# Performance work log

Hardware: AMD Instinct MI355X
Metric: run time of the kernel (lower is better)

The kernel has to match this reference:

```python
import jax, jax.numpy as jnp
import numpy as np

B, T, C, H, HS = 64, 128, 4096, 32, 128  # T must equal HS = C // H (source code constraint)
SCALE = 32.0 ** -0.5  # fixed constant in source, NOT head_size**-0.5


def setup_inputs() -> dict:
    key = jax.random.key(0)
    ks = jax.random.split(key, 6)
    s = 0.02
    return {
        "x": jax.random.normal(ks[0], (B, T, C), dtype=jnp.float32),
        "wq": jax.random.normal(ks[1], (H, C, HS), dtype=jnp.float32) * s,
        "wk": jax.random.normal(ks[2], (H, C, HS), dtype=jnp.float32) * s,
        "wv": jax.random.normal(ks[3], (H, C, HS), dtype=jnp.float32) * s,
        "wp": jax.random.normal(ks[4], (C, C), dtype=jnp.float32) * s,
        "bp": jnp.zeros((C,), dtype=jnp.float32),
    }


def reference(x, wq, wk, wv, wp, bp):
    # Batched per-head projections (source loops over heads; math identical).
    q = jnp.einsum("btc,hcs->bhts", x, wq)  # [B,H,T,HS]
    k = jnp.einsum("btc,hcs->bhts", x, wk)
    v = jnp.einsum("btc,hcs->bhts", x, wv)
    wei = jnp.einsum("bhts,bhus->bhtu", q, k) * SCALE  # [B,H,Tq,Tk]
    # Source uses F.softmax(wei, dim=1) on [B,Tq,Tk] -> softmax over QUERY axis.
    wei = jax.nn.softmax(wei, axis=2)
    out = jnp.einsum("bhtu,bhus->bhts", wei, v)  # [B,H,T,HS]
    # torch.cat(dim=1) over heads -> [B, H*T, HS]; then transpose(1,2) -> [B, HS, H*T]
    out = out.reshape(B, H * T, HS).transpose(0, 2, 1)  # [B, HS, H*T]; H*T == C
    out = jnp.einsum("bse,oe->bso", out, wp) + bp  # proj Linear
    return out  # dropout is identity in eval mode
```

## Files before the change

kernel.cpp:

```cpp
#include <hip/hip_runtime.h>
#include <cstddef>
#include <cstdint>

#define NB 64
#define NH 32
#define NT 128
#define NHS 128
#define NC 4096
#define SCALE 0.17677669529663687f
#define SLD 136

typedef __bf16 bf16_t;
typedef __bf16 bf16x8 __attribute__((ext_vector_type(8)));
typedef float  f32x4  __attribute__((ext_vector_type(4)));

__device__ __forceinline__ void load_lds16(const bf16_t* g, bf16_t* l) {
    __builtin_amdgcn_global_load_lds(
        (const __attribute__((address_space(1))) char*)g,
        (__attribute__((address_space(3))) char*)l,
        16, 0, 0);
}

__global__ __launch_bounds__(256) void cvt_bf16_kernel(
    const float* __restrict__ in, bf16_t* __restrict__ out, int n8)
{
    int i = blockIdx.x * 256 + threadIdx.x;
    if (i >= n8) return;
    const float4* p = (const float4*)in + (size_t)i * 2;
    float4 a = p[0], b = p[1];
    bf16x8 o;
    o[0] = (bf16_t)a.x; o[1] = (bf16_t)a.y; o[2] = (bf16_t)a.z; o[3] = (bf16_t)a.w;
    o[4] = (bf16_t)b.x; o[5] = (bf16_t)b.y; o[6] = (bf16_t)b.z; o[7] = (bf16_t)b.w;
    ((bf16x8*)out)[i] = o;
}

__global__ __launch_bounds__(256) void cvt_w_transpose_kernel(
    const float* __restrict__ wq, const float* __restrict__ wk, const float* __restrict__ wv,
    bf16_t* __restrict__ qt, bf16_t* __restrict__ kt, bf16_t* __restrict__ vt)
{
    const float* w; bf16_t* o;
    if (blockIdx.y == 0)      { w = wq; o = qt; }
    else if (blockIdx.y == 1) { w = wk; o = kt; }
    else                      { w = wv; o = vt; }
    const int h   = blockIdx.x >> 7;
    const int rem = blockIdx.x & 127;
    const int c0  = (rem >> 1) * 64;
    const int s0  = (rem & 1) * 64;
    const float* W = w + (size_t)h * NC * NHS;
    bf16_t* O = o + (size_t)h * NHS * NC;

    __shared__ float t[64][65];
    const int tid = threadIdx.x;
    #pragma unroll
    for (int it = 0; it < 16; ++it) {
        int idx = it * 256 + tid;
        int r = idx >> 6, cc = idx & 63;
        t[r][cc] = W[(size_t)(c0 + r) * NHS + s0 + cc];
    }
    __syncthreads();
    #pragma unroll
    for (int it = 0; it < 16; ++it) {
        int idx = it * 256 + tid;
        int sr = idx >> 6, cr = idx & 63;
        O[(size_t)(s0 + sr) * NC + c0 + cr] = (bf16_t)t[cr][sr];
    }
}

#define TILE_EL 16384

__device__ __forceinline__ void gemm256_core(
    const bf16_t* __restrict__ A, const bf16_t* __restrict__ BT, f32x4 acc[8][4])
{
    __shared__ __align__(16) bf16_t As[2 * TILE_EL];
    __shared__ __align__(16) bf16_t Bs[2 * TILE_EL];

    const int tid  = threadIdx.x;
    const int lane = tid & 63;
    const int w    = tid >> 6;
    const int wr   = w >> 2;
    const int wc   = w & 3;

    const int srow  = tid >> 3;
    const int scol  = ((tid & 7) * 8) ^ (((tid >> 3) & 7) << 3);
    const int sslot = tid * 8;

    const int frow = lane & 15;
    const int fk   = (lane >> 4) * 8;
    int aoff[2][2][4];
    #pragma unroll
    for (int ks = 0; ks < 2; ++ks)
        #pragma unroll
        for (int mh = 0; mh < 2; ++mh)
            #pragma unroll
            for (int q = 0; q < 4; ++q) {
                int r = wr * 128 + mh * 64 + q * 16 + frow;
                aoff[ks][mh][q] = r * 64 + ((ks * 32 + fk) ^ ((r & 7) << 3));
            }
    int boff[2][4];
    #pragma unroll
    for (int ks = 0; ks < 2; ++ks)
        #pragma unroll
        for (int n = 0; n < 4; ++n) {
            int r = wc * 64 + n * 16 + frow;
            boff[ks][n] = r * 64 + ((ks * 32 + fk) ^ ((r & 7) << 3));
        }

    auto stage = [&](const bf16_t* __restrict__ G, int half, int k0, bf16_t* dst) {
        #pragma unroll
        for (int jj = 0; jj < 2; ++jj) {
            const int j = half * 2 + jj;
            load_lds16(G + (size_t)(j * 64 + srow) * NC + (k0 + scol),
                       dst + j * 4096 + sslot);
        }
    };

    stage(A,  0, 0, As);           stage(A,  1, 0, As);
    stage(BT, 0, 0, Bs);           stage(BT, 1, 0, Bs);
    stage(A,  0, 64, As + TILE_EL); stage(A,  1, 64, As + TILE_EL);
    stage(BT, 0, 64, Bs + TILE_EL); stage(BT, 1, 64, Bs + TILE_EL);
    asm volatile("s_waitcnt vmcnt(8)" ::: "memory");
    __builtin_amdgcn_s_barrier();
    __builtin_amdgcn_sched_barrier(0);

    for (int t = 0; t < NC / 64; ++t) {
        bf16_t* Ac = As + (t & 1) * TILE_EL;
        bf16_t* Bc = Bs + (t & 1) * TILE_EL;
        const int  kn = t * 64 + 128;
        const bool pf = (t < NC / 64 - 2);

        bf16x8 b0[4], b1[4], a[4];
        #pragma unroll
        for (int n = 0; n < 4; ++n) b0[n] = *(const bf16x8*)(Bc + boff[0][n]);
        #pragma unroll
        for (int n = 0; n < 4; ++n) b1[n] = *(const bf16x8*)(Bc + boff[1][n]);
        #pragma unroll
        for (int q = 0; q < 4; ++q) a[q] = *(const bf16x8*)(Ac + aoff[0][0][q]);
        __builtin_amdgcn_s_setprio(1);
        #pragma unroll
        for (int q = 0; q < 4; ++q)
            #pragma unroll
            for (int n = 0; n < 4; ++n)
                acc[q][n] = __builtin_amdgcn_mfma_f32_16x16x32_bf16(a[q], b0[n], acc[q][n], 0, 0, 0);
        __builtin_amdgcn_s_setprio(0);
        asm volatile("s_waitcnt lgkmcnt(0)" ::: "memory");
        __builtin_amdgcn_s_barrier();
        __builtin_amdgcn_sched_barrier(0);

        if (pf) stage(BT, 0, kn, Bc);
        #pragma unroll
        for (int q = 0; q < 4; ++q) a[q] = *(const bf16x8*)(Ac + aoff[0][1][q]);
        __builtin_amdgcn_s_setprio(1);
        #pragma unroll
        for (int q = 0; q < 4; ++q)
            #pragma unroll
            for (int n = 0; n < 4; ++n)
                acc[4 + q][n] = __builtin_amdgcn_mfma_f32_16x16x32_bf16(a[q], b0[n], acc[4 + q][n], 0, 0, 0);
        __builtin_amdgcn_s_setprio(0);

        if (pf) stage(BT, 1, kn, Bc);
        #pragma unroll
        for (int q = 0; q < 4; ++q) a[q] = *(const bf16x8*)(Ac + aoff[1][0][q]);
        __builtin_amdgcn_s_setprio(1);
        #pragma unroll
        for (int q = 0; q < 4; ++q)
            #pragma unroll
            for (int n = 0; n < 4; ++n)
                acc[q][n] = __builtin_amdgcn_mfma_f32_16x16x32_bf16(a[q], b1[n], acc[q][n], 0, 0, 0);
        __builtin_amdgcn_s_setprio(0);

        #pragma unroll
        for (int q = 0; q < 4; ++q) a[q] = *(const bf16x8*)(Ac + aoff[1][1][q]);
        __builtin_amdgcn_s_setprio(1);
        #pragma unroll
        for (int q = 0; q < 4; ++q)
            #pragma unroll
            for (int n = 0; n < 4; ++n)
                acc[4 + q][n] = __builtin_amdgcn_mfma_f32_16x16x32_bf16(a[q], b1[n], acc[4 + q][n], 0, 0, 0);
        __builtin_amdgcn_s_setprio(0);

        asm volatile("s_waitcnt lgkmcnt(0)" ::: "memory");
        __builtin_amdgcn_s_barrier();
        __builtin_amdgcn_sched_barrier(0);
        if (pf) {
            stage(A, 0, kn, Ac); stage(A, 1, kn, Ac);
            asm volatile("s_waitcnt vmcnt(8)" ::: "memory");
        } else if (t == NC / 64 - 2) {
            asm volatile("s_waitcnt vmcnt(0)" ::: "memory");
        }
        __builtin_amdgcn_s_barrier();
        __builtin_amdgcn_sched_barrier(0);
    }
}

__global__ __launch_bounds__(512, 2) void qkv_gemm256_kernel(
    const bf16_t* __restrict__ xb, const bf16_t* __restrict__ wcat,
    bf16_t* __restrict__ q, bf16_t* __restrict__ k, bf16_t* __restrict__ v)
{
    const int bid = blockIdx.x;
    const int wg  = (bid & 7) * 192 + (bid >> 3);
    const int mt  = wg / 48;
    const int nt  = wg - mt * 48;
    const int Mb  = mt << 8;
    const int Nb  = nt << 8;

    f32x4 acc[8][4] = {};
    gemm256_core(xb + (size_t)Mb * NC, wcat + (size_t)Nb * NC, acc);

    const int tid = threadIdx.x, lane = tid & 63, w = tid >> 6;
    const int wr = w >> 2, wc = w & 3;
    const int tens = Nb >> 12;
    bf16_t* const outp = (tens == 0) ? q : (tens == 1) ? k : v;
    const int colb = Nb + wc * 64 + (lane & 15);
    const int rowb = Mb + wr * 128 + ((lane >> 4) << 2);
    #pragma unroll
    for (int i = 0; i < 8; ++i)
        #pragma unroll
        for (int r = 0; r < 4; ++r) {
            const int m  = rowb + i * 16 + r;
            const int bb = m >> 7, tt = m & 127;
            #pragma unroll
            for (int n = 0; n < 4; ++n) {
                const int ng = colb + n * 16;
                const int hh = (ng >> 7) & 31, ss = ng & 127;
                const size_t base = (size_t)((bb << 5) + hh) << 14;
                if (tens == 2) outp[base + ss * NT  + tt] = (bf16_t)acc[i][n][r];
                else           outp[base + tt * NHS + ss] = (bf16_t)acc[i][n][r];
            }
        }
}

__global__ __launch_bounds__(512, 2) void proj_gemm256_kernel(
    const bf16_t* __restrict__ attnT, const bf16_t* __restrict__ wpb,
    const float* __restrict__ bp, float* __restrict__ out)
{
    const int bid = blockIdx.x;
    const int wg  = (bid & 7) * 64 + (bid >> 3);
    const int mt  = wg >> 4;
    const int nt  = wg & 15;
    const int Mb  = mt << 8;
    const int Nb  = nt << 8;

    f32x4 acc[8][4] = {};
    gemm256_core(attnT + (size_t)Mb * NC, wpb + (size_t)Nb * NC, acc);

    const int tid = threadIdx.x, lane = tid & 63, w = tid >> 6;
    const int wr = w >> 2, wc = w & 3;
    const int colb = Nb + wc * 64 + (lane & 15);
    const int rowb = Mb + wr * 128 + ((lane >> 4) << 2);
    float bias[4];
    #pragma unroll
    for (int n = 0; n < 4; ++n) bias[n] = bp[colb + n * 16];
    #pragma unroll
    for (int i = 0; i < 8; ++i)
        #pragma unroll
        for (int r = 0; r < 4; ++r) {
            const size_t m = (size_t)(rowb + i * 16 + r);
            #pragma unroll
            for (int n = 0; n < 4; ++n)
                out[m * NC + colb + n * 16] = acc[i][n][r] + bias[n];
        }
}

__global__ __launch_bounds__(256) void attn_mfma_kernel(
    const bf16_t* __restrict__ q, const bf16_t* __restrict__ k,
    const bf16_t* __restrict__ vT, bf16_t* __restrict__ attnT)
{
    __shared__ __align__(16) bf16_t As[128 * 32];
    __shared__ __align__(16) bf16_t Bs[128 * 32];
    __shared__ __align__(16) bf16_t S[NT * SLD];

    const int bh = blockIdx.x;
    const int b = bh >> 5, h = bh & 31;
    const bf16_t* Q  = q  + (size_t)bh * NT * NHS;
    const bf16_t* K  = k  + (size_t)bh * NT * NHS;
    const bf16_t* VT = vT + (size_t)bh * NT * NHS;

    const int tid  = threadIdx.x;
    const int lane = tid & 63;
    const int wave = tid >> 6;
    const int wr = (wave >> 1) * 64;
    const int wc = (wave & 1) * 64;
    const int srow = tid >> 2;
    const int scol = (tid & 3) * 8;
    const int m0 = wr + (lane & 15);
    const int n0 = wc + (lane & 15);
    const int kq = (lane >> 4) * 8;
    const int rbase = wr + (lane >> 4) * 4;

    f32x4 acc[4][4] = {};

    for (int k0 = 0; k0 < NHS; k0 += 32) {
        load_lds16(Q + (size_t)srow        * NHS + k0 + scol, &As[srow * 32 + scol]);
        load_lds16(Q + (size_t)(srow + 64) * NHS + k0 + scol, &As[(srow + 64) * 32 + scol]);
        load_lds16(K + (size_t)srow        * NHS + k0 + scol, &Bs[srow * 32 + scol]);
        load_lds16(K + (size_t)(srow + 64) * NHS + k0 + scol, &Bs[(srow + 64) * 32 + scol]);
        __syncthreads();
        bf16x8 af[4], bfr[4];
        #pragma unroll
        for (int i = 0; i < 4; ++i) af[i]  = *(const bf16x8*)&As[(m0 + i * 16) * 32 + kq];
        #pragma unroll
        for (int j = 0; j < 4; ++j) bfr[j] = *(const bf16x8*)&Bs[(n0 + j * 16) * 32 + kq];
        #pragma unroll
        for (int i = 0; i < 4; ++i)
            #pragma unroll
            for (int j = 0; j < 4; ++j)
                acc[i][j] = __builtin_amdgcn_mfma_f32_16x16x32_bf16(af[i], bfr[j], acc[i][j], 0, 0, 0);
        __syncthreads();
    }
    #pragma unroll
    for (int i = 0; i < 4; ++i)
        #pragma unroll
        for (int j = 0; j < 4; ++j)
            #pragma unroll
            for (int r = 0; r < 4; ++r)
                S[(rbase + i * 16 + r) * SLD + wc + j * 16 + (lane & 15)] =
                    (bf16_t)(acc[i][j][r] * SCALE);
    __syncthreads();

    if (tid < NT) {
        const int u = tid;
        float m = -1e30f;
        for (int t = 0; t < NT; ++t) m = fmaxf(m, (float)S[t * SLD + u]);
        float sum = 0.f;
        for (int t = 0; t < NT; ++t) sum += __expf((float)S[t * SLD + u] - m);
        const float inv = 1.0f / sum;
        for (int t = 0; t < NT; ++t)
            S[t * SLD + u] = (bf16_t)(__expf((float)S[t * SLD + u] - m) * inv);
    }
    __syncthreads();

    #pragma unroll
    for (int i = 0; i < 4; ++i)
        #pragma unroll
        for (int j = 0; j < 4; ++j)
            acc[i][j] = (f32x4)(0.0f);

    for (int k0 = 0; k0 < NT; k0 += 32) {
        load_lds16(VT + (size_t)srow        * NT + k0 + scol, &As[srow * 32 + scol]);
        load_lds16(VT + (size_t)(srow + 64) * NT + k0 + scol, &As[(srow + 64) * 32 + scol]);
        __syncthreads();
        bf16x8 af[4], bfr[4];
        #pragma unroll
        for (int i = 0; i < 4; ++i) af[i]  = *(const bf16x8*)&As[(m0 + i * 16) * 32 + kq];
        #pragma unroll
        for (int j = 0; j < 4; ++j) bfr[j] = *(const bf16x8*)&S[(n0 + j * 16) * SLD + k0 + kq];
        #pragma unroll
        for (int i = 0; i < 4; ++i)
            #pragma unroll
            for (int j = 0; j < 4; ++j)
                acc[i][j] = __builtin_amdgcn_mfma_f32_16x16x32_bf16(af[i], bfr[j], acc[i][j], 0, 0, 0);
        __syncthreads();
    }
    bf16_t* AT = attnT + (size_t)b * NHS * NC + h * NT;
    #pragma unroll
    for (int i = 0; i < 4; ++i)
        #pragma unroll
        for (int j = 0; j < 4; ++j)
            #pragma unroll
            for (int r = 0; r < 4; ++r)
                AT[(size_t)(rbase + i * 16 + r) * NC + wc + j * 16 + (lane & 15)] =
                    (bf16_t)acc[i][j][r];
}

extern "C" void kernel_launch(void* const* d_in, const int* in_sizes, int n_in,
                              void* d_out, int out_size, void* d_ws, size_t ws_size,
                              hipStream_t stream) {
    const float* x  = (const float*)d_in[0];
    const float* wq = (const float*)d_in[1];
    const float* wk = (const float*)d_in[2];
    const float* wv = (const float*)d_in[3];
    const float* wp = (const float*)d_in[4];
    const float* bp = (const float*)d_in[5];
    float* out = (float*)d_out;

    const size_t NX = (size_t)NB * NT * NC;
    const size_t NW = (size_t)NH * NC * NHS;
    bf16_t* xb  = (bf16_t*)d_ws;
    bf16_t* wqT = xb  + NX;
    bf16_t* wkT = wqT + NW;
    bf16_t* wvT = wkT + NW;
    bf16_t* wpb = wvT + NW;
    bf16_t* qb  = wpb + NW;
    bf16_t* kb  = qb  + NX;
    bf16_t* vb  = kb  + NX;
    bf16_t* atT = vb  + NX;

    cvt_bf16_kernel<<<(int)(NX / 8 / 256), 256, 0, stream>>>(x, xb, (int)(NX / 8));
    cvt_w_transpose_kernel<<<dim3(4096, 3), 256, 0, stream>>>(wq, wk, wv, wqT, wkT, wvT);
    cvt_bf16_kernel<<<(int)(NW / 8 / 256), 256, 0, stream>>>(wp, wpb, (int)(NW / 8));

    qkv_gemm256_kernel<<<1536, 512, 0, stream>>>(xb, wqT, qb, kb, vb);
    attn_mfma_kernel<<<NB * NH, 256, 0, stream>>>(qb, kb, vb, atT);
    proj_gemm256_kernel<<<512, 512, 0, stream>>>(atT, wpb, bp, out);
}
```

Baseline: 1.648 ms.

## Triple-buffer A tiles and restructure GEMM loop into barrier-separated phases

Result: faster. 1.597 ms (-3.1%).

```diff
diff --git a/kernel.cpp b/kernel.cpp
--- a/kernel.cpp
+++ b/kernel.cpp
@@ -66,13 +66,13 @@
     }
 }
 
-#define TILE_EL 16384
+#define KT_EL 16384
 
 __device__ __forceinline__ void gemm256_core(
     const bf16_t* __restrict__ A, const bf16_t* __restrict__ BT, f32x4 acc[8][4])
 {
-    __shared__ __align__(16) bf16_t As[2 * TILE_EL];
-    __shared__ __align__(16) bf16_t Bs[2 * TILE_EL];
+    __shared__ __align__(16) bf16_t As[3 * KT_EL];
+    __shared__ __align__(16) bf16_t Bs[2 * KT_EL];
 
     const int tid  = threadIdx.x;
     const int lane = tid & 63;
@@ -90,11 +90,11 @@
     #pragma unroll
     for (int ks = 0; ks < 2; ++ks)
         #pragma unroll
-        for (int mh = 0; mh < 2; ++mh)
+        for (int ih = 0; ih < 2; ++ih)
             #pragma unroll
             for (int q = 0; q < 4; ++q) {
-                int r = wr * 128 + mh * 64 + q * 16 + frow;
-                aoff[ks][mh][q] = r * 64 + ((ks * 32 + fk) ^ ((r & 7) << 3));
+                int r = wr * 128 + ih * 64 + q * 16 + frow;
+                aoff[ks][ih][q] = r * 64 + ((ks * 32 + fk) ^ ((r & 7) << 3));
             }
     int boff[2][4];
     #pragma unroll
@@ -105,7 +105,7 @@
             boff[ks][n] = r * 64 + ((ks * 32 + fk) ^ ((r & 7) << 3));
         }
 
-    auto stage = [&](const bf16_t* __restrict__ G, int half, int k0, bf16_t* dst) {
+    auto stageH = [&](const bf16_t* __restrict__ G, int half, int k0, bf16_t* dst) {
         #pragma unroll
         for (int jj = 0; jj < 2; ++jj) {
             const int j = half * 2 + jj;
@@ -114,27 +114,37 @@
         }
     };
 
-    stage(A,  0, 0, As);           stage(A,  1, 0, As);
-    stage(BT, 0, 0, Bs);           stage(BT, 1, 0, Bs);
-    stage(A,  0, 64, As + TILE_EL); stage(A,  1, 64, As + TILE_EL);
-    stage(BT, 0, 64, Bs + TILE_EL); stage(BT, 1, 64, Bs + TILE_EL);
-    asm volatile("s_waitcnt vmcnt(8)" ::: "memory");
+    stageH(BT, 0, 0, Bs);          stageH(BT, 1, 0, Bs);
+    stageH(A,  0, 0, As);          stageH(A,  1, 0, As);
+    stageH(A,  0, 64, As + KT_EL); stageH(A,  1, 64, As + KT_EL);
+    asm volatile("s_waitcnt vmcnt(4)" ::: "memory");
     __builtin_amdgcn_s_barrier();
     __builtin_amdgcn_sched_barrier(0);
 
+    int a_cur = 0;
+    #pragma unroll 1
     for (int t = 0; t < NC / 64; ++t) {
-        bf16_t* Ac = As + (t & 1) * TILE_EL;
-        bf16_t* Bc = Bs + (t & 1) * TILE_EL;
-        const int  kn = t * 64 + 128;
-        const bool pf = (t < NC / 64 - 2);
-
-        bf16x8 b0[4], b1[4], a[4];
+        bf16_t* Ac = As + a_cur * KT_EL;
+        bf16_t* Bc = Bs + (t & 1) * KT_EL;
+        bf16_t* Bn = Bs + ((t + 1) & 1) * KT_EL;
+        const int a_n2 = (a_cur >= 1) ? a_cur - 1 : 2;
+        bf16_t* An = As + a_n2 * KT_EL;
+        const bool pfB = (t < NC / 64 - 1);
+        const bool pfA = (t < NC / 64 - 2);
+        const int kB = (t + 1) * 64;
+        const int kA = (t + 2) * 64;
+
+        bf16x8 a[4], b0[4], b1[4];
+
         #pragma unroll
         for (int n = 0; n < 4; ++n) b0[n] = *(const bf16x8*)(Bc + boff[0][n]);
         #pragma unroll
-        for (int n = 0; n < 4; ++n) b1[n] = *(const bf16x8*)(Bc + boff[1][n]);
-        #pragma unroll
         for (int q = 0; q < 4; ++q) a[q] = *(const bf16x8*)(Ac + aoff[0][0][q]);
+        if (pfB) stageH(BT, 0, kB, Bn);
+        __builtin_amdgcn_sched_barrier(0);
+        __builtin_amdgcn_s_barrier();
+        asm volatile("s_waitcnt lgkmcnt(0)" ::: "memory");
+        __builtin_amdgcn_sched_barrier(0);
         __builtin_amdgcn_s_setprio(1);
         #pragma unroll
         for (int q = 0; q < 4; ++q)
@@ -142,13 +152,16 @@
             for (int n = 0; n < 4; ++n)
                 acc[q][n] = __builtin_amdgcn_mfma_f32_16x16x32_bf16(a[q], b0[n], acc[q][n], 0, 0, 0);
         __builtin_amdgcn_s_setprio(0);
+        __builtin_amdgcn_s_barrier();
+        __builtin_amdgcn_sched_barrier(0);
+
+        #pragma unroll
+        for (int q = 0; q < 4; ++q) a[q] = *(const bf16x8*)(Ac + aoff[0][1][q]);
+        if (pfB) stageH(BT, 1, kB, Bn);
+        __builtin_amdgcn_sched_barrier(0);
+        __builtin_amdgcn_s_barrier();
         asm volatile("s_waitcnt lgkmcnt(0)" ::: "memory");
-        __builtin_amdgcn_s_barrier();
-        __builtin_amdgcn_sched_barrier(0);
-
-        if (pf) stage(BT, 0, kn, Bc);
-        #pragma unroll
-        for (int q = 0; q < 4; ++q) a[q] = *(const bf16x8*)(Ac + aoff[0][1][q]);
+        __builtin_amdgcn_sched_barrier(0);
         __builtin_amdgcn_s_setprio(1);
         #pragma unroll
         for (int q = 0; q < 4; ++q)
@@ -156,10 +169,18 @@
             for (int n = 0; n < 4; ++n)
                 acc[4 + q][n] = __builtin_amdgcn_mfma_f32_16x16x32_bf16(a[q], b0[n], acc[4 + q][n], 0, 0, 0);
         __builtin_amdgcn_s_setprio(0);
-
-        if (pf) stage(BT, 1, kn, Bc);
+        __builtin_amdgcn_s_barrier();
+        __builtin_amdgcn_sched_barrier(0);
+
+        #pragma unroll
+        for (int n = 0; n < 4; ++n) b1[n] = *(const bf16x8*)(Bc + boff[1][n]);
         #pragma unroll
         for (int q = 0; q < 4; ++q) a[q] = *(const bf16x8*)(Ac + aoff[1][0][q]);
+        if (pfA) stageH(A, 0, kA, An);
+        __builtin_amdgcn_sched_barrier(0);
+        __builtin_amdgcn_s_barrier();
+        asm volatile("s_waitcnt lgkmcnt(0)" ::: "memory");
+        __builtin_amdgcn_sched_barrier(0);
         __builtin_amdgcn_s_setprio(1);
         #pragma unroll
         for (int q = 0; q < 4; ++q)
@@ -167,9 +188,21 @@
             for (int n = 0; n < 4; ++n)
                 acc[q][n] = __builtin_amdgcn_mfma_f32_16x16x32_bf16(a[q], b1[n], acc[q][n], 0, 0, 0);
         __builtin_amdgcn_s_setprio(0);
+        __builtin_amdgcn_s_barrier();
+        __builtin_amdgcn_sched_barrier(0);
 
         #pragma unroll
         for (int q = 0; q < 4; ++q) a[q] = *(const bf16x8*)(Ac + aoff[1][1][q]);
+        if (pfA) {
+            stageH(A, 1, kA, An);
+            asm volatile("s_waitcnt vmcnt(4)" ::: "memory");
+        } else if (pfB) {
+            asm volatile("s_waitcnt vmcnt(0)" ::: "memory");
+        }
+        __builtin_amdgcn_sched_barrier(0);
+        __builtin_amdgcn_s_barrier();
+        asm volatile("s_waitcnt lgkmcnt(0)" ::: "memory");
+        __builtin_amdgcn_sched_barrier(0);
         __builtin_amdgcn_s_setprio(1);
         #pragma unroll
         for (int q = 0; q < 4; ++q)
@@ -177,18 +210,10 @@
             for (int n = 0; n < 4; ++n)
                 acc[4 + q][n] = __builtin_amdgcn_mfma_f32_16x16x32_bf16(a[q], b1[n], acc[4 + q][n], 0, 0, 0);
         __builtin_amdgcn_s_setprio(0);
-
-        asm volatile("s_waitcnt lgkmcnt(0)" ::: "memory");
-        __builtin_amdgcn_s_barrier();
-        __builtin_amdgcn_sched_barrier(0);
-        if (pf) {
-            stage(A, 0, kn, Ac); stage(A, 1, kn, Ac);
-            asm volatile("s_waitcnt vmcnt(8)" ::: "memory");
-        } else if (t == NC / 64 - 2) {
-            asm volatile("s_waitcnt vmcnt(0)" ::: "memory");
-        }
-        __builtin_amdgcn_s_barrier();
-        __builtin_amdgcn_sched_barrier(0);
+        __builtin_amdgcn_s_barrier();
+        __builtin_amdgcn_sched_barrier(0);
+
+        a_cur = (a_cur == 2) ? 0 : a_cur + 1;
     }
 }
 
```

## Restructure GEMM main loop into four-phase ping-pong schedule and vectorize V stores

Applied to the files above, without the earlier changes.

Measured after the change: 1.659 ms. About the same (+0.7%).

```diff
diff --git a/kernel.cpp b/kernel.cpp
--- a/kernel.cpp
+++ b/kernel.cpp
@@ -20,6 +20,10 @@
         (__attribute__((address_space(3))) char*)l,
         16, 0, 0);
 }
+
+#define SBAR() __builtin_amdgcn_sched_barrier(0)
+#define BARRIER() __builtin_amdgcn_s_barrier()
+#define LGKM0() asm volatile("s_waitcnt lgkmcnt(0)" ::: "memory")
 
 __global__ __launch_bounds__(256) void cvt_bf16_kernel(
     const float* __restrict__ in, bf16_t* __restrict__ out, int n8)
@@ -66,13 +70,13 @@
     }
 }
 
-#define TILE_EL 16384
+#define KT_EL 16384
 
 __device__ __forceinline__ void gemm256_core(
     const bf16_t* __restrict__ A, const bf16_t* __restrict__ BT, f32x4 acc[8][4])
 {
-    __shared__ __align__(16) bf16_t As[2 * TILE_EL];
-    __shared__ __align__(16) bf16_t Bs[2 * TILE_EL];
+    __shared__ __align__(16) bf16_t As[2 * KT_EL];
+    __shared__ __align__(16) bf16_t Bs[2 * KT_EL];
 
     const int tid  = threadIdx.x;
     const int lane = tid & 63;
@@ -90,11 +94,11 @@
     #pragma unroll
     for (int ks = 0; ks < 2; ++ks)
         #pragma unroll
-        for (int mh = 0; mh < 2; ++mh)
+        for (int ih = 0; ih < 2; ++ih)
             #pragma unroll
             for (int q = 0; q < 4; ++q) {
-                int r = wr * 128 + mh * 64 + q * 16 + frow;
-                aoff[ks][mh][q] = r * 64 + ((ks * 32 + fk) ^ ((r & 7) << 3));
+                int r = wr * 128 + ih * 64 + q * 16 + frow;
+                aoff[ks][ih][q] = r * 64 + ((ks * 32 + fk) ^ ((r & 7) << 3));
             }
     int boff[2][4];
     #pragma unroll
@@ -105,90 +109,148 @@
             boff[ks][n] = r * 64 + ((ks * 32 + fk) ^ ((r & 7) << 3));
         }
 
-    auto stage = [&](const bf16_t* __restrict__ G, int half, int k0, bf16_t* dst) {
-        #pragma unroll
-        for (int jj = 0; jj < 2; ++jj) {
-            const int j = half * 2 + jj;
-            load_lds16(G + (size_t)(j * 64 + srow) * NC + (k0 + scol),
-                       dst + j * 4096 + sslot);
-        }
+    auto stageS = [&](const bf16_t* __restrict__ G, int j, int k0, bf16_t* dst) {
+        load_lds16(G + (size_t)(j * 64 + srow) * NC + (k0 + scol),
+                   dst + j * 4096 + sslot);
     };
-
-    stage(A,  0, 0, As);           stage(A,  1, 0, As);
-    stage(BT, 0, 0, Bs);           stage(BT, 1, 0, Bs);
-    stage(A,  0, 64, As + TILE_EL); stage(A,  1, 64, As + TILE_EL);
-    stage(BT, 0, 64, Bs + TILE_EL); stage(BT, 1, 64, Bs + TILE_EL);
-    asm volatile("s_waitcnt vmcnt(8)" ::: "memory");
-    __builtin_amdgcn_s_barrier();
-    __builtin_amdgcn_sched_barrier(0);
-
-    for (int t = 0; t < NC / 64; ++t) {
-        bf16_t* Ac = As + (t & 1) * TILE_EL;
-        bf16_t* Bc = Bs + (t & 1) * TILE_EL;
-        const int  kn = t * 64 + 128;
-        const bool pf = (t < NC / 64 - 2);
-
-        bf16x8 b0[4], b1[4], a[4];
-        #pragma unroll
-        for (int n = 0; n < 4; ++n) b0[n] = *(const bf16x8*)(Bc + boff[0][n]);
-        #pragma unroll
-        for (int n = 0; n < 4; ++n) b1[n] = *(const bf16x8*)(Bc + boff[1][n]);
-        #pragma unroll
-        for (int q = 0; q < 4; ++q) a[q] = *(const bf16x8*)(Ac + aoff[0][0][q]);
+    auto stageH = [&](const bf16_t* __restrict__ G, int half, int k0, bf16_t* dst) {
+        #pragma unroll
+        for (int jj = 0; jj < 2; ++jj)
+            stageS(G, half * 2 + jj, k0, dst);
+    };
+
+    stageH(A,  0, 0, As);  stageH(A,  1, 0, As);
+    stageH(BT, 0, 0, Bs);  stageH(BT, 1, 0, Bs);
+    stageS(A, 0, 64, As + KT_EL);
+    stageS(A, 2, 64, As + KT_EL);
+    stageH(BT, 0, 64, Bs + KT_EL);
+    stageH(BT, 1, 64, Bs + KT_EL);
+    asm volatile("s_waitcnt vmcnt(6)" ::: "memory");
+    BARRIER();
+    SBAR();
+
+    bf16x8 b0c[2][2];
+    #pragma unroll
+    for (int ks = 0; ks < 2; ++ks)
+        #pragma unroll
+        for (int n = 0; n < 2; ++n)
+            b0c[ks][n] = *(const bf16x8*)(Bs + boff[ks][n]);
+
+    #pragma unroll 1
+    for (int t = 0; t < 64; ++t) {
+        const int p = t & 1;
+        bf16_t* Ac = As + p * KT_EL;
+        bf16_t* Bc = Bs + p * KT_EL;
+        bf16_t* Ao = As + (p ^ 1) * KT_EL;
+        bf16_t* Bo = Bs + (p ^ 1) * KT_EL;
+        const bool s1 = (t < 63);
+        const bool s2 = (t < 62);
+        const int k1 = (t + 1) * 64;
+        const int k2 = (t + 2) * 64;
+
+        bf16x8 a0[2][4], a1[2][4], b1[2][2], b0n[2][2];
+
+        #pragma unroll
+        for (int ks = 0; ks < 2; ++ks)
+            #pragma unroll
+            for (int q = 0; q < 4; ++q)
+                a0[ks][q] = *(const bf16x8*)(Ac + aoff[ks][0][q]);
+        if (s1) { stageS(A, 1, k1, Ao); stageS(A, 3, k1, Ao); }
+        SBAR();
+        BARRIER();
+        LGKM0();
+        SBAR();
         __builtin_amdgcn_s_setprio(1);
         #pragma unroll
-        for (int q = 0; q < 4; ++q)
-            #pragma unroll
-            for (int n = 0; n < 4; ++n)
-                acc[q][n] = __builtin_amdgcn_mfma_f32_16x16x32_bf16(a[q], b0[n], acc[q][n], 0, 0, 0);
+        for (int ks = 0; ks < 2; ++ks)
+            #pragma unroll
+            for (int q = 0; q < 4; ++q)
+                #pragma unroll
+                for (int n = 0; n < 2; ++n)
+                    acc[q][n] = __builtin_amdgcn_mfma_f32_16x16x32_bf16(a0[ks][q], b0c[ks][n], acc[q][n], 0, 0, 0);
         __builtin_amdgcn_s_setprio(0);
-        asm volatile("s_waitcnt lgkmcnt(0)" ::: "memory");
-        __builtin_amdgcn_s_barrier();
-        __builtin_amdgcn_sched_barrier(0);
-
-        if (pf) stage(BT, 0, kn, Bc);
-        #pragma unroll
-        for (int q = 0; q < 4; ++q) a[q] = *(const bf16x8*)(Ac + aoff[0][1][q]);
+        BARRIER();
+        SBAR();
+
+        #pragma unroll
+        for (int ks = 0; ks < 2; ++ks)
+            #pragma unroll
+            for (int n = 0; n < 2; ++n)
+                b1[ks][n] = *(const bf16x8*)(Bc + boff[ks][2 + n]);
+        if (s2) { stageS(A, 0, k2, Ac); stageS(A, 2, k2, Ac); }
+        SBAR();
+        BARRIER();
+        LGKM0();
+        SBAR();
         __builtin_amdgcn_s_setprio(1);
         #pragma unroll
-        for (int q = 0; q < 4; ++q)
-            #pragma unroll
-            for (int n = 0; n < 4; ++n)
-                acc[4 + q][n] = __builtin_amdgcn_mfma_f32_16x16x32_bf16(a[q], b0[n], acc[4 + q][n], 0, 0, 0);
+        for (int ks = 0; ks < 2; ++ks)
+            #pragma unroll
+            for (int q = 0; q < 4; ++q)
+                #pragma unroll
+                for (int n = 0; n < 2; ++n)
+                    acc[q][2 + n] = __builtin_amdgcn_mfma_f32_16x16x32_bf16(a0[ks][q], b1[ks][n], acc[q][2 + n], 0, 0, 0);
         __builtin_amdgcn_s_setprio(0);
-
-        if (pf) stage(BT, 1, kn, Bc);
-        #pragma unroll
-        for (int q = 0; q < 4; ++q) a[q] = *(const bf16x8*)(Ac + aoff[1][0][q]);
+        BARRIER();
+        SBAR();
+
+        #pragma unroll
+        for (int ks = 0; ks < 2; ++ks)
+            #pragma unroll
+            for (int q = 0; q < 4; ++q)
+                a1[ks][q] = *(const bf16x8*)(Ac + aoff[ks][1][q]);
+        if (s2) stageH(BT, 0, k2, Bc);
+        SBAR();
+        BARRIER();
+        LGKM0();
+        SBAR();
         __builtin_amdgcn_s_setprio(1);
         #pragma unroll
-        for (int q = 0; q < 4; ++q)
-            #pragma unroll
-            for (int n = 0; n < 4; ++n)
-                acc[q][n] = __builtin_amdgcn_mfma_f32_16x16x32_bf16(a[q], b1[n], acc[q][n], 0, 0, 0);
+        for (int ks = 0; ks < 2; ++ks)
+            #pragma unroll
+            for (int q = 0; q < 4; ++q)
+                #pragma unroll
+                for (int n = 0; n < 2; ++n)
+                    acc[4 + q][2 + n] = __builtin_amdgcn_mfma_f32_16x16x32_bf16(a1[ks][q], b1[ks][n], acc[4 + q][2 + n], 0, 0, 0);
         __builtin_amdgcn_s_setprio(0);
-
-        #pragma unroll
-        for (int q = 0; q < 4; ++q) a[q] = *(const bf16x8*)(Ac + aoff[1][1][q]);
+        BARRIER();
+        SBAR();
+
+        if (s2) {
+            stageH(BT, 1, k2, Bc);
+            asm volatile("s_waitcnt vmcnt(6)" ::: "memory");
+        } else if (t == 62) {
+            asm volatile("s_waitcnt vmcnt(0)" ::: "memory");
+        }
+        SBAR();
+        BARRIER();
+        SBAR();
         __builtin_amdgcn_s_setprio(1);
         #pragma unroll
-        for (int q = 0; q < 4; ++q)
-            #pragma unroll
-            for (int n = 0; n < 4; ++n)
-                acc[4 + q][n] = __builtin_amdgcn_mfma_f32_16x16x32_bf16(a[q], b1[n], acc[4 + q][n], 0, 0, 0);
+        for (int ks = 0; ks < 2; ++ks)
+            #pragma unroll
+            for (int q = 0; q < 4; ++q)
+                #pragma unroll
+                for (int n = 0; n < 2; ++n)
+                    acc[4 + q][n] = __builtin_amdgcn_mfma_f32_16x16x32_bf16(a1[ks][q], b0c[ks][n], acc[4 + q][n], 0, 0, 0);
         __builtin_amdgcn_s_setprio(0);
-
-        asm volatile("s_waitcnt lgkmcnt(0)" ::: "memory");
-        __builtin_amdgcn_s_barrier();
-        __builtin_amdgcn_sched_barrier(0);
-        if (pf) {
-            stage(A, 0, kn, Ac); stage(A, 1, kn, Ac);
-            asm volatile("s_waitcnt vmcnt(8)" ::: "memory");
-        } else if (t == NC / 64 - 2) {
-            asm volatile("s_waitcnt vmcnt(0)" ::: "memory");
-        }
-        __builtin_amdgcn_s_barrier();
-        __builtin_amdgcn_sched_barrier(0);
+        if (s1) {
+            #pragma unroll
+            for (int ks = 0; ks < 2; ++ks)
+                #pragma unroll
+                for (int n = 0; n < 2; ++n)
+                    b0n[ks][n] = *(const bf16x8*)(Bo + boff[ks][n]);
+        }
+        SBAR();
+        BARRIER();
+        SBAR();
+        if (s1) {
+            #pragma unroll
+            for (int ks = 0; ks < 2; ++ks)
+                #pragma unroll
+                for (int n = 0; n < 2; ++n)
+                    b0c[ks][n] = b0n[ks][n];
+        }
     }
 }
 
@@ -212,21 +274,38 @@
     bf16_t* const outp = (tens == 0) ? q : (tens == 1) ? k : v;
     const int colb = Nb + wc * 64 + (lane & 15);
     const int rowb = Mb + wr * 128 + ((lane >> 4) << 2);
-    #pragma unroll
-    for (int i = 0; i < 8; ++i)
-        #pragma unroll
-        for (int r = 0; r < 4; ++r) {
-            const int m  = rowb + i * 16 + r;
-            const int bb = m >> 7, tt = m & 127;
+    if (tens == 2) {
+        #pragma unroll
+        for (int i = 0; i < 8; ++i) {
+            const int m0 = rowb + i * 16;
+            const int bb = m0 >> 7, tt0 = m0 & 127;
             #pragma unroll
             for (int n = 0; n < 4; ++n) {
                 const int ng = colb + n * 16;
                 const int hh = (ng >> 7) & 31, ss = ng & 127;
                 const size_t base = (size_t)((bb << 5) + hh) << 14;
-                if (tens == 2) outp[base + ss * NT  + tt] = (bf16_t)acc[i][n][r];
-                else           outp[base + tt * NHS + ss] = (bf16_t)acc[i][n][r];
+                bf16_t pk[4];
+                #pragma unroll
+                for (int r = 0; r < 4; ++r) pk[r] = (bf16_t)acc[i][n][r];
+                *(uint64_t*)(outp + base + (size_t)ss * NT + tt0) = *(const uint64_t*)pk;
             }
         }
+    } else {
+        #pragma unroll
+        for (int i = 0; i < 8; ++i)
+            #pragma unroll
+            for (int r = 0; r < 4; ++r) {
+                const int m  = rowb + i * 16 + r;
+                const int bb = m >> 7, tt = m & 127;
+                #pragma unroll
+                for (int n = 0; n < 4; ++n) {
+                    const int ng = colb + n * 16;
+                    const int hh = (ng >> 7) & 31, ss = ng & 127;
+                    const size_t base = (size_t)((bb << 5) + hh) << 14;
+                    outp[base + (size_t)tt * NHS + ss] = (bf16_t)acc[i][n][r];
+                }
+            }
+    }
 }
 
 __global__ __launch_bounds__(512, 2) void proj_gemm256_kernel(
```
